# Performance work log

Measured on AMD Instinct MI355X. Metric: run time of the kernel, lower is better.

The kernel has to match this reference:

```python
import jax, jax.numpy as jnp
import numpy as np

L = 100  # hidden size of lstm1 (module hardcodes self.L = 100)


def _lstm_cell(x, h, c, W_ih, W_hh, b_ih, b_hh):
    # PyTorch LSTMCell: gates ordered (input, forget, cell, output)
    gates = x @ W_ih.T + h @ W_hh.T + b_ih + b_hh  # [B, 4*H]
    i, f, g, o = jnp.split(gates, 4, axis=-1)
    i = jax.nn.sigmoid(i)
    f = jax.nn.sigmoid(f)
    g = jnp.tanh(g)
    o = jax.nn.sigmoid(o)
    c_new = f * c + i * g
    h_new = o * jnp.tanh(c_new)
    return h_new, c_new


def setup_inputs() -> dict:
    key = jax.random.key(0)
    ks = jax.random.split(key, 9)
    B, T = 4096, 2048
    s1 = 1.0 / np.sqrt(L)   # torch LSTMCell init scale for hidden 100
    s2 = 1.0                # hidden size 1 -> scale 1
    return {
        "input": jax.random.normal(ks[0], (B, T), dtype=jnp.float32),
        "W_ih1": jax.random.uniform(ks[1], (4 * L, 1), jnp.float32, -s1, s1),
        "W_hh1": jax.random.uniform(ks[2], (4 * L, L), jnp.float32, -s1, s1),
        "b_ih1": jax.random.uniform(ks[3], (4 * L,), jnp.float32, -s1, s1),
        "b_hh1": jax.random.uniform(ks[4], (4 * L,), jnp.float32, -s1, s1),
        "W_ih2": jax.random.uniform(ks[5], (4, L), jnp.float32, -s2, s2),
        "W_hh2": jax.random.uniform(ks[6], (4, 1), jnp.float32, -s2, s2),
        "b_ih2": jax.random.uniform(ks[7], (4,), jnp.float32, -s2, s2),
        "b_hh2": jax.random.uniform(ks[8], (4,), jnp.float32, -s2, s2),
    }


def reference(input, W_ih1, W_hh1, b_ih1, b_hh1, W_ih2, W_hh2, b_ih2, b_hh2):
    B, T = input.shape
    x_seq = input.T[:, :, None]  # [T, B, 1]
    h1 = jnp.zeros((B, L), input.dtype)
    c1 = jnp.zeros((B, L), input.dtype)
    h2 = jnp.zeros((B, 1), input.dtype)
    c2 = jnp.zeros((B, 1), input.dtype)

    def step(carry, x_t):
        h1, c1, h2, c2 = carry
        h1, c1 = _lstm_cell(x_t, h1, c1, W_ih1, W_hh1, b_ih1, b_hh1)
        h2, c2 = _lstm_cell(h1, h2, c2, W_ih2, W_hh2, b_ih2, b_hh2)
        return (h1, c1, h2, c2), h2  # emit h2: [B, 1]

    _, outs = jax.lax.scan(step, (h1, c1, h2, c2), x_seq)
    # outs: [T, B, 1] -> stack along time dim then squeeze, matching torch.stack(.,1).squeeze(2)
    return outs[:, :, 0].T  # [B, T]
```

## Files before the change

### kernel.cpp

```cpp
#include <hip/hip_runtime.h>
#include <math.h>

#define BB 4096
#define TT 2048
#define LL 100

constexpr int NB = 16;
constexpr int WG = 448;
constexpr int KT = 7;

#define L2E 1.44269504088896340736f

#define AG(kt, row) (((kt) * 64 + ((row) ^ ((row) >> 3))) * 4)

typedef short bf16x8 __attribute__((ext_vector_type(8)));
typedef float f32x4 __attribute__((ext_vector_type(4)));

union AF { int4 v; bf16x8 f; unsigned int w[4]; };

__device__ __forceinline__ float frcp(float x) { return __builtin_amdgcn_rcpf(x); }
__device__ __forceinline__ float fexp2(float x) {
#if __has_builtin(__builtin_amdgcn_exp2f)
    return __builtin_amdgcn_exp2f(x);
#else
    return exp2f(x);
#endif
}
__device__ __forceinline__ float sig2(float xp) { return frcp(1.0f + fexp2(-xp)); }
__device__ __forceinline__ float th2(float xpp) { return 1.0f - 2.0f * frcp(1.0f + fexp2(xpp)); }
__device__ __forceinline__ float ftanh_n(float x) { return th2(2.0f * L2E * x); }

__device__ __forceinline__ unsigned int cvt_pk_bf16(float lo, float hi) {
    unsigned int d;
    asm("v_cvt_pk_bf16_f32 %0, %1, %2" : "=v"(d) : "v"(lo), "v"(hi));
    return d;
}

__global__ void __launch_bounds__(WG)
__attribute__((amdgpu_waves_per_eu(2, 2)))
lstm2_kernel(const float* __restrict__ input,
             const float* __restrict__ W_ih1,
             const float* __restrict__ W_hh1,
             const float* __restrict__ b_ih1,
             const float* __restrict__ b_hh1,
             const float* __restrict__ W_ih2,
             const float* __restrict__ W_hh2,
             const float* __restrict__ b_ih2,
             const float* __restrict__ b_hh2,
             float* __restrict__ out)
{
    __shared__ __align__(16) unsigned int afrag[2][KT * 256];

    const int tid = threadIdx.x;
    const int wave = tid >> 6;
    const int lane = tid & 63;
    const int col16 = lane & 15;
    const int quad = lane >> 4;
    const int bg0 = blockIdx.x * NB;

    for (int i = tid; i < 2 * KT * 256; i += WG) (&afrag[0][0])[i] = 0u;

    const int sb = (wave == 3) ? 6 : ((wave < 3) ? wave : wave - 1);
    const int uu = 16 * sb + col16;
    const bool uvalid = (uu < LL);
    const bool l2lane = (wave == 3) && (col16 == 8);
    const bool xlane = (wave == 3) && (col16 == 4);
    const bool wr_en = (uu <= 100);

    const float gsc[4] = {L2E, L2E, 2.0f * L2E, L2E};

    bf16x8 bb[4][KT];
#pragma unroll
    for (int g = 0; g < 4; ++g)
#pragma unroll
        for (int kt = 0; kt < KT; ++kt)
#pragma unroll
            for (int j = 0; j < 8; ++j) {
                const int k = 32 * kt + 8 * quad + j;
                const int i = k >> 1;
                float w = 0.0f;
                if (i < LL) {
                    if (l2lane)       w = W_ih2[g * LL + i] * gsc[g];
                    else if (uvalid)  w = W_hh1[(100 * g + uu) * LL + i] * gsc[g];
                } else if (i == 100) {
                    if (!l2lane && uvalid) w = W_ih1[100 * g + uu] * gsc[g];
                }
                const unsigned int hh = cvt_pk_bf16(w, 0.0f) & 0xffffu;
                if (!(k & 1)) {
                    bb[g][kt][j] = (short)hh;
                } else {
                    const float wres = w - __uint_as_float(hh << 16);
                    bb[g][kt][j] = (short)(cvt_pk_bf16(wres, 0.0f) & 0xffffu);
                }
            }

    f32x4 binit[4];
#pragma unroll
    for (int g = 0; g < 4; ++g) {
        float bv = 0.0f;
        if (l2lane)      bv = (b_ih2[g] + b_hh2[g]) * gsc[g];
        else if (uvalid) bv = (b_ih1[100 * g + uu] + b_hh1[100 * g + uu]) * gsc[g];
        binit[g] = (f32x4){bv, bv, bv, bv};
    }

    float c1[4] = {0.f, 0.f, 0.f, 0.f};

    int wofs[4];
#pragma unroll
    for (int r = 0; r < 4; ++r) {
        const int row = 4 * quad + r + 16 * ((col16 >> 2) & 3);
        wofs[r] = AG(sb, row) + (col16 & 3);
    }

    float wh2s[4], h2v[4] = {0.f, 0.f, 0.f, 0.f}, c2v[4] = {0.f, 0.f, 0.f, 0.f};
#pragma unroll
    for (int g = 0; g < 4; ++g)
        wh2s[g] = l2lane ? W_hh2[g] * gsc[g] : 0.0f;

    __syncthreads();

    if (xlane) {
#pragma unroll
        for (int r = 0; r < 4; ++r) {
            const int m = 4 * quad + r;
            const float x0 = input[(size_t)(bg0 + m) * TT];
            const unsigned int hh = cvt_pk_bf16(x0, x0);
            const float hf = __uint_as_float(hh << 16);
            afrag[0][wofs[r]] = cvt_pk_bf16(x0, x0 - hf);
        }
    }
    __syncthreads();

    for (int t = 0; t <= TT; ++t) {
        const int p = t & 1, pn = p ^ 1;

        if (t < TT || wave == 3) {
            float xnext[4] = {0.f, 0.f, 0.f, 0.f};
            if (xlane && t + 1 < TT) {
#pragma unroll
                for (int r = 0; r < 4; ++r)
                    xnext[r] = input[(size_t)(bg0 + 4 * quad + r) * TT + (t + 1)];
            }

            AF a[KT];
#pragma unroll
            for (int kt = 0; kt < KT; ++kt)
                a[kt].v = *(const int4*)&afrag[p][AG(kt, lane)];

            f32x4 acc[4];
#pragma unroll
            for (int g = 0; g < 4; ++g)
                acc[g] = __builtin_amdgcn_mfma_f32_16x16x32_bf16(a[0].f, bb[g][0], binit[g], 0, 0, 0);
#pragma unroll
            for (int kt = 1; kt < KT; ++kt)
#pragma unroll
                for (int g = 0; g < 4; ++g)
                    acc[g] = __builtin_amdgcn_mfma_f32_16x16x32_bf16(a[kt].f, bb[g][kt], acc[g], 0, 0, 0);

            if (l2lane && t >= 1) {
#pragma unroll
                for (int r = 0; r < 4; ++r) {
                    const float p0 = fmaf(wh2s[0], h2v[r], acc[0][r]);
                    const float p1 = fmaf(wh2s[1], h2v[r], acc[1][r]);
                    const float p2 = fmaf(wh2s[2], h2v[r], acc[2][r]);
                    const float p3 = fmaf(wh2s[3], h2v[r], acc[3][r]);
                    const float i2 = sig2(p0), f2 = sig2(p1), g2 = th2(p2), o2 = sig2(p3);
                    c2v[r] = f2 * c2v[r] + i2 * g2;
                    h2v[r] = o2 * ftanh_n(c2v[r]);
                    out[(size_t)(bg0 + 4 * quad + r) * TT + (t - 1)] = h2v[r];
                }
            }

            if (t < TT) {
#pragma unroll
                for (int r = 0; r < 4; ++r) {
                    const float iv = sig2(acc[0][r]);
                    const float fv = sig2(acc[1][r]);
                    const float gv = th2(acc[2][r]);
                    const float ov = sig2(acc[3][r]);
                    const float c = fv * c1[r] + iv * gv;
                    c1[r] = c;
                    const float h = uvalid ? (ov * ftanh_n(c)) : xnext[r];
                    if (wr_en) {
                        const unsigned int hh = cvt_pk_bf16(h, h);
                        const float hf = __uint_as_float(hh << 16);
                        afrag[pn][wofs[r]] = cvt_pk_bf16(h, h - hf);
                    }
                }
            }
        }

        __syncthreads();
    }
}

extern "C" void kernel_launch(void* const* d_in, const int* in_sizes, int n_in,
                              void* d_out, int out_size, void* d_ws, size_t ws_size,
                              hipStream_t stream) {
    const float* input = (const float*)d_in[0];
    const float* W_ih1 = (const float*)d_in[1];
    const float* W_hh1 = (const float*)d_in[2];
    const float* b_ih1 = (const float*)d_in[3];
    const float* b_hh1 = (const float*)d_in[4];
    const float* W_ih2 = (const float*)d_in[5];
    const float* W_hh2 = (const float*)d_in[6];
    const float* b_ih2 = (const float*)d_in[7];
    const float* b_hh2 = (const float*)d_in[8];
    float* out = (float*)d_out;

    dim3 grid(BB / NB);
    dim3 block(WG);
    lstm2_kernel<<<grid, block, 0, stream>>>(input, W_ih1, W_hh1, b_ih1, b_hh1,
                                             W_ih2, W_hh2, b_ih2, b_hh2, out);
}
```

Baseline: 2.322 ms.

## Pack two hidden-unit tiles per wave with four waves per workgroup

Reduces the workgroup from 7 waves to 4. Waves 0-2 now each compute two 16-unit tiles (A and B), and wave 3 handles tile 6 plus the layer-2 and input lanes. The aim is to cut the per-step __syncthreads cost across fewer waves and reuse the loaded A fragments for twice the MFMA work per wave. The cost is doubled B-operand registers per wave, with occupancy pinned to one wave per EU, so the serial MFMA chain per wave gets longer and wave 3 carries an uneven load.

```diff
diff --git a/kernel.cpp b/kernel.cpp
--- a/kernel.cpp
+++ b/kernel.cpp
@@ -6,7 +6,7 @@
 #define LL 100
 
 constexpr int NB = 16;
-constexpr int WG = 448;
+constexpr int WG = 256;
 constexpr int KT = 7;
 
 #define L2E 1.44269504088896340736f
@@ -37,7 +37,7 @@
 }
 
 __global__ void __launch_bounds__(WG)
-__attribute__((amdgpu_waves_per_eu(2, 2)))
+__attribute__((amdgpu_waves_per_eu(1, 1)))
 lstm2_kernel(const float* __restrict__ input,
              const float* __restrict__ W_ih1,
              const float* __restrict__ W_hh1,
@@ -60,16 +60,19 @@
 
     for (int i = tid; i < 2 * KT * 256; i += WG) (&afrag[0][0])[i] = 0u;
 
-    const int sb = (wave == 3) ? 6 : ((wave < 3) ? wave : wave - 1);
-    const int uu = 16 * sb + col16;
-    const bool uvalid = (uu < LL);
+    const int tA = (wave == 3) ? 6 : wave;
+    const int tB = wave + 3;
+    const bool hasB = (wave < 3);
+    const int uuA = 16 * tA + col16;
+    const int uuB = 16 * tB + col16;
+    const bool uvalidA = (uuA < LL);
     const bool l2lane = (wave == 3) && (col16 == 8);
     const bool xlane = (wave == 3) && (col16 == 4);
-    const bool wr_en = (uu <= 100);
+    const bool wrA = (uuA <= 100);
 
     const float gsc[4] = {L2E, L2E, 2.0f * L2E, L2E};
 
-    bf16x8 bb[4][KT];
+    bf16x8 bbA[4][KT], bbB[4][KT];
 #pragma unroll
     for (int g = 0; g < 4; ++g)
 #pragma unroll
@@ -78,38 +81,51 @@
             for (int j = 0; j < 8; ++j) {
                 const int k = 32 * kt + 8 * quad + j;
                 const int i = k >> 1;
-                float w = 0.0f;
+                float wA = 0.0f;
                 if (i < LL) {
-                    if (l2lane)       w = W_ih2[g * LL + i] * gsc[g];
-                    else if (uvalid)  w = W_hh1[(100 * g + uu) * LL + i] * gsc[g];
+                    if (l2lane)        wA = W_ih2[g * LL + i] * gsc[g];
+                    else if (uvalidA)  wA = W_hh1[(100 * g + uuA) * LL + i] * gsc[g];
                 } else if (i == 100) {
-                    if (!l2lane && uvalid) w = W_ih1[100 * g + uu] * gsc[g];
-                }
-                const unsigned int hh = cvt_pk_bf16(w, 0.0f) & 0xffffu;
+                    if (!l2lane && uvalidA) wA = W_ih1[100 * g + uuA] * gsc[g];
+                }
+                float wB = 0.0f;
+                if (hasB) {
+                    if (i < LL)        wB = W_hh1[(100 * g + uuB) * LL + i] * gsc[g];
+                    else if (i == 100) wB = W_ih1[100 * g + uuB] * gsc[g];
+                }
+                const unsigned int hA = cvt_pk_bf16(wA, 0.0f) & 0xffffu;
+                const unsigned int hB = cvt_pk_bf16(wB, 0.0f) & 0xffffu;
                 if (!(k & 1)) {
-                    bb[g][kt][j] = (short)hh;
+                    bbA[g][kt][j] = (short)hA;
+                    bbB[g][kt][j] = (short)hB;
                 } else {
-                    const float wres = w - __uint_as_float(hh << 16);
-                    bb[g][kt][j] = (short)(cvt_pk_bf16(wres, 0.0f) & 0xffffu);
-                }
-            }
-
-    f32x4 binit[4];
+                    const float rA = wA - __uint_as_float(hA << 16);
+                    const float rB = wB - __uint_as_float(hB << 16);
+                    bbA[g][kt][j] = (short)(cvt_pk_bf16(rA, 0.0f) & 0xffffu);
+                    bbB[g][kt][j] = (short)(cvt_pk_bf16(rB, 0.0f) & 0xffffu);
+                }
+            }
+
+    f32x4 binitA[4], binitB[4];
 #pragma unroll
     for (int g = 0; g < 4; ++g) {
-        float bv = 0.0f;
-        if (l2lane)      bv = (b_ih2[g] + b_hh2[g]) * gsc[g];
-        else if (uvalid) bv = (b_ih1[100 * g + uu] + b_hh1[100 * g + uu]) * gsc[g];
-        binit[g] = (f32x4){bv, bv, bv, bv};
-    }
-
-    float c1[4] = {0.f, 0.f, 0.f, 0.f};
-
-    int wofs[4];
+        float bA = 0.0f, bB = 0.0f;
+        if (l2lane)       bA = (b_ih2[g] + b_hh2[g]) * gsc[g];
+        else if (uvalidA) bA = (b_ih1[100 * g + uuA] + b_hh1[100 * g + uuA]) * gsc[g];
+        if (hasB)         bB = (b_ih1[100 * g + uuB] + b_hh1[100 * g + uuB]) * gsc[g];
+        binitA[g] = (f32x4){bA, bA, bA, bA};
+        binitB[g] = (f32x4){bB, bB, bB, bB};
+    }
+
+    float c1A[4] = {0.f, 0.f, 0.f, 0.f};
+    float c1B[4] = {0.f, 0.f, 0.f, 0.f};
+
+    int wofsA[4], wofsB[4];
 #pragma unroll
     for (int r = 0; r < 4; ++r) {
-        const int row = 4 * quad + r + 16 * ((col16 >> 2) & 3);
-        wofs[r] = AG(sb, row) + (col16 & 3);
+        const int row = 4 * quad + r + 16 * (col16 >> 2);
+        wofsA[r] = AG(tA, row) + (col16 & 3);
+        wofsB[r] = AG(tB, row) + (col16 & 3);
     }
 
     float wh2s[4], h2v[4] = {0.f, 0.f, 0.f, 0.f}, c2v[4] = {0.f, 0.f, 0.f, 0.f};
@@ -126,7 +142,7 @@
             const float x0 = input[(size_t)(bg0 + m) * TT];
             const unsigned int hh = cvt_pk_bf16(x0, x0);
             const float hf = __uint_as_float(hh << 16);
-            afrag[0][wofs[r]] = cvt_pk_bf16(x0, x0 - hf);
+            afrag[0][wofsA[r]] = cvt_pk_bf16(x0, x0 - hf);
         }
     }
     __syncthreads();
@@ -147,23 +163,34 @@
             for (int kt = 0; kt < KT; ++kt)
                 a[kt].v = *(const int4*)&afrag[p][AG(kt, lane)];
 
-            f32x4 acc[4];
+            f32x4 accA[4], accB[4];
 #pragma unroll
             for (int g = 0; g < 4; ++g)
-                acc[g] = __builtin_amdgcn_mfma_f32_16x16x32_bf16(a[0].f, bb[g][0], binit[g], 0, 0, 0);
+                accA[g] = __builtin_amdgcn_mfma_f32_16x16x32_bf16(a[0].f, bbA[g][0], binitA[g], 0, 0, 0);
 #pragma unroll
             for (int kt = 1; kt < KT; ++kt)
 #pragma unroll
                 for (int g = 0; g < 4; ++g)
-                    acc[g] = __builtin_amdgcn_mfma_f32_16x16x32_bf16(a[kt].f, bb[g][kt], acc[g], 0, 0, 0);
+                    accA[g] = __builtin_amdgcn_mfma_f32_16x16x32_bf16(a[kt].f, bbA[g][kt], accA[g], 0, 0, 0);
+
+            if (hasB) {
+#pragma unroll
+                for (int g = 0; g < 4; ++g)
+                    accB[g] = __builtin_amdgcn_mfma_f32_16x16x32_bf16(a[0].f, bbB[g][0], binitB[g], 0, 0, 0);
+#pragma unroll
+                for (int kt = 1; kt < KT; ++kt)
+#pragma unroll
+                    for (int g = 0; g < 4; ++g)
+                        accB[g] = __builtin_amdgcn_mfma_f32_16x16x32_bf16(a[kt].f, bbB[g][kt], accB[g], 0, 0, 0);
+            }
 
             if (l2lane && t >= 1) {
 #pragma unroll
                 for (int r = 0; r < 4; ++r) {
-                    const float p0 = fmaf(wh2s[0], h2v[r], acc[0][r]);
-                    const float p1 = fmaf(wh2s[1], h2v[r], acc[1][r]);
-                    const float p2 = fmaf(wh2s[2], h2v[r], acc[2][r]);
-                    const float p3 = fmaf(wh2s[3], h2v[r], acc[3][r]);
+                    const float p0 = fmaf(wh2s[0], h2v[r], accA[0][r]);
+                    const float p1 = fmaf(wh2s[1], h2v[r], accA[1][r]);
+                    const float p2 = fmaf(wh2s[2], h2v[r], accA[2][r]);
+                    const float p3 = fmaf(wh2s[3], h2v[r], accA[3][r]);
                     const float i2 = sig2(p0), f2 = sig2(p1), g2 = th2(p2), o2 = sig2(p3);
                     c2v[r] = f2 * c2v[r] + i2 * g2;
                     h2v[r] = o2 * ftanh_n(c2v[r]);
@@ -174,17 +201,32 @@
             if (t < TT) {
 #pragma unroll
                 for (int r = 0; r < 4; ++r) {
-                    const float iv = sig2(acc[0][r]);
-                    const float fv = sig2(acc[1][r]);
-                    const float gv = th2(acc[2][r]);
-                    const float ov = sig2(acc[3][r]);
-                    const float c = fv * c1[r] + iv * gv;
-                    c1[r] = c;
-                    const float h = uvalid ? (ov * ftanh_n(c)) : xnext[r];
-                    if (wr_en) {
+                    const float iv = sig2(accA[0][r]);
+                    const float fv = sig2(accA[1][r]);
+                    const float gv = th2(accA[2][r]);
+                    const float ov = sig2(accA[3][r]);
+                    const float c = fv * c1A[r] + iv * gv;
+                    c1A[r] = c;
+                    const float h = uvalidA ? (ov * ftanh_n(c)) : xnext[r];
+                    if (wrA) {
                         const unsigned int hh = cvt_pk_bf16(h, h);
                         const float hf = __uint_as_float(hh << 16);
-                        afrag[pn][wofs[r]] = cvt_pk_bf16(h, h - hf);
+                        afrag[pn][wofsA[r]] = cvt_pk_bf16(h, h - hf);
+                    }
+                }
+                if (hasB) {
+#pragma unroll
+                    for (int r = 0; r < 4; ++r) {
+                        const float iv = sig2(accB[0][r]);
+                        const float fv = sig2(accB[1][r]);
+                        const float gv = th2(accB[2][r]);
+                        const float ov = sig2(accB[3][r]);
+                        const float c = fv * c1B[r] + iv * gv;
+                        c1B[r] = c;
+                        const float h = ov * ftanh_n(c);
+                        const unsigned int hh = cvt_pk_bf16(h, h);
+                        const float hf = __uint_as_float(hh << 16);
+                        afrag[pn][wofsB[r]] = cvt_pk_bf16(h, h - hf);
                     }
                 }
             }
```

New measurement: 2.849 ms. 1.23x slower.
